# Kernel tuning notes

Hardware: AMD Instinct MI355X
Metric: run time of the kernel (lower is better)

## Reference

```python
import jax, jax.numpy as jnp
import numpy as np

NH = 8  # n_heads
LN_EPS = 1e-5

def _ln(x, g, b):
    m = x.mean(-1, keepdims=True)
    v = ((x - m) ** 2).mean(-1, keepdims=True)
    return (x - m) / jnp.sqrt(v + LN_EPS) * g + b

def _l2norm(x):
    n = jnp.sqrt(jnp.sum(x * x, axis=-1, keepdims=True))
    return x / jnp.maximum(n, 1e-12)

def _block(h, inw, inb, outw, outb, g1, b1, g2, b2, w1, bb1, w2, bb2):
    B, T, D = h.shape
    hd = D // NH
    res = h
    hn = _ln(h, g1, b1)
    qkv = hn @ inw.T + inb
    q, k, v = jnp.split(qkv, 3, axis=-1)
    q = q.reshape(B, T, NH, hd)
    k = k.reshape(B, T, NH, hd)
    v = v.reshape(B, T, NH, hd)
    scores = jnp.einsum('bthd,bshd->bhts', q, k) / jnp.sqrt(jnp.asarray(hd, h.dtype))
    a = jax.nn.softmax(scores, axis=-1)
    o = jnp.einsum('bhts,bshd->bthd', a, v).reshape(B, T, D)
    h = res + o @ outw.T + outb
    f = _ln(h, g2, b2)
    f = jax.nn.gelu(f @ w1.T + bb1, approximate=False) @ w2.T + bb2
    return h + f

def setup_inputs() -> dict:
    B, T, IN, D, L, NS, NP = 8, 1024, 1024, 512, 4, 1024, 512
    key = jax.random.key(0)
    ks = jax.random.split(key, 24)
    gn = jax.random.normal
    u = jax.random.uniform(ks[1], (B, T, NS), dtype=jnp.float32, minval=1e-6, maxval=1.0 - 1e-6)
    gumbel = -jnp.log(-jnp.log(u))
    s = lambda fan: 1.0 / np.sqrt(fan)
    inp = {
        'x': gn(ks[0], (B, T, IN), dtype=jnp.float32),
        'gumbel': gumbel,
        'sym_w': gn(ks[2], (D, IN)) * s(IN),
        'sym_b': jnp.zeros((D,)),
        'codebook': gn(ks[3], (NS, D)) * 0.1,
        'pos_enc': gn(ks[4], (1, 2000, D)) * 0.02,
        'attn_in_w': gn(ks[5], (L, 3 * D, D)) * s(D),
        'attn_in_b': jnp.zeros((L, 3 * D)),
        'attn_out_w': gn(ks[6], (L, D, D)) * s(D),
        'attn_out_b': jnp.zeros((L, D)),
        'n1_g': jnp.ones((L, D)), 'n1_b': jnp.zeros((L, D)),
        'n2_g': jnp.ones((L, D)), 'n2_b': jnp.zeros((L, D)),
        'ffn_w1': gn(ks[7], (L, 4 * D, D)) * s(D),
        'ffn_b1': jnp.zeros((L, 4 * D)),
        'ffn_w2': gn(ks[8], (L, D, 4 * D)) * s(4 * D),
        'ffn_b2': jnp.zeros((L, D)),
        'q_w': gn(ks[9], (D, D)) * s(D),
        'q_b': jnp.zeros((D,)),
        'qln_g': jnp.ones((D,)), 'qln_b': jnp.zeros((D,)),
        'patterns': gn(ks[10], (NP, D)) * s(D),
        'epoch': 0,
        'total_epochs': 100,
    }
    return inp

def reference(x, gumbel, sym_w, sym_b, codebook, pos_enc,
              attn_in_w, attn_in_b, attn_out_w, attn_out_b,
              n1_g, n1_b, n2_g, n2_b, ffn_w1, ffn_b1, ffn_w2, ffn_b2,
              q_w, q_b, qln_g, qln_b, patterns, epoch, total_epochs):
    B, T, _ = x.shape
    # SymbolizationLayer (soft, gumbel-softmax with tau=0.5)
    hp = x @ sym_w.T + sym_b                               # [B,T,D]
    logits_s = _l2norm(hp) @ _l2norm(codebook).T / 0.5     # [B,T,NS]
    soft = jax.nn.softmax((logits_s + gumbel) / 0.5, axis=-1)
    h = soft @ codebook + pos_enc[:, :T, :]
    # transformer blocks
    for i in range(attn_in_w.shape[0]):
        h = _block(h, attn_in_w[i], attn_in_b[i], attn_out_w[i], attn_out_b[i],
                   n1_g[i], n1_b[i], n2_g[i], n2_b[i],
                   ffn_w1[i], ffn_b1[i], ffn_w2[i], ffn_b2[i])
    # VQPatternMatrix (eval mode: hard assignments, no EMA updates)
    Q = _l2norm(_ln(h @ q_w.T + q_b, qln_g, qln_b))
    temp = max(0.5, 1.0 - 0.5 * epoch / total_epochs)
    logits = Q @ _l2norm(patterns).T / temp                # [B,T,NP]
    hard_idx = jnp.argmax(logits, axis=-1)                 # [B,T]
    assign = jax.nn.one_hot(hard_idx, patterns.shape[0], dtype=logits.dtype)
    emb = jnp.take(patterns, hard_idx, axis=0)             # gather = one_hot @ patterns
    return (emb, assign, logits, h, hard_idx)
```

## Files before the change

### kernel.cpp

```cpp
#include <hip/hip_runtime.h>

#define DEV __device__ __forceinline__

typedef unsigned short u16;
typedef unsigned int u32;
typedef __attribute__((ext_vector_type(8))) _Float16 h8_t;
typedef __attribute__((ext_vector_type(4))) float f4_t;

constexpr int T_SEQ = 1024;
constexpr int DMODEL = 512;
constexpr int NPAT = 512;

enum {
  E_BIAS = 0,
  E_VQ = 5,
  E_RES = 6,
  E_ACC = 7,
  E_POS = 8,
  E_GUM2 = 9,
  E_GELU2 = 10,
  E_QKV2 = 11
};

DEV float h2f(u16 h) { return (float)__builtin_bit_cast(_Float16, h); }
DEV void split2(float x, u16& h, u16& l) {
  _Float16 hh = (_Float16)x;
  float r = x - (float)hh;
  _Float16 ll = (_Float16)r;
  h = __builtin_bit_cast(u16, hh);
  l = __builtin_bit_cast(u16, ll);
}

DEV f4_t mfh(h8_t a, h8_t b, f4_t c) {
  return __builtin_amdgcn_mfma_f32_16x16x32_f16(a, b, c, 0, 0, 0);
}
DEV f4_t prod3(h8_t ah, h8_t al, h8_t bh, h8_t bl, f4_t c) {
  c = mfh(ah, bh, c);
  c = mfh(ah, bl, c);
  c = mfh(al, bh, c);
  return c;
}

typedef const __attribute__((address_space(1))) unsigned char* gas_t;
typedef __attribute__((address_space(3))) unsigned char* las_t;
DEV void gload16(const u16* g, u16* l) {
  __builtin_amdgcn_global_load_lds((gas_t)(const void*)g, (las_t)(void*)l, 16,
                                   0, 0);
}

template <int EPI>
__global__ __launch_bounds__(256, 3) void gemm_mf(
    const u16* __restrict__ Ah, const u16* __restrict__ Al,
    const u16* __restrict__ Bh, const u16* __restrict__ Bl,
    const float* __restrict__ bias, const float* __restrict__ res,
    float* __restrict__ Cf, u16* __restrict__ Ch, u16* __restrict__ Cl, int N,
    int KK, int lda, int ldb, int gx) {
  constexpr int BM = 64;
  constexpr int MT = 2;
  __shared__ __align__(16) u16 AsH[2][BM][4][8], AsL[2][BM][4][8];
  __shared__ __align__(16) u16 BsH[2][128][4][8], BsL[2][128][4][8];
  const int tid = threadIdx.x;
  const int w = tid >> 6, lane = tid & 63;
  const int wy = w >> 1, wx = w & 1;
  const int lr = lane & 15, lg = lane >> 4;

  const int nwg = gridDim.x;
  const int bid = blockIdx.x;
  const int qq = nwg >> 3;
  const int wg = (bid & 7) * qq + (bid >> 3);
  const int by = wg / gx, bx = wg % gx;
  const int bm = by * BM, bn = bx * 128;

  const int rowl = lane >> 2, slot4 = lane & 3;

  auto STAGE = [&](int k0, int buf) {
#pragma unroll
    for (int it = 0; it < 2; ++it) {
      const int f = w + 4 * it;
      const int plane = f >> 2;
      const int ch = f & 3;
      const int row = ch * 16 + rowl;
      const int kp = slot4 ^ ((row >> 1) & 3);
      const size_t g = (size_t)(bm + row) * lda + k0 + kp * 8;
      if (plane == 0)
        gload16(&Ah[g], &AsH[buf][0][0][0] + ch * 512);
      else
        gload16(&Al[g], &AsL[buf][0][0][0] + ch * 512);
    }
#pragma unroll
    for (int it = 0; it < 4; ++it) {
      const int f = w + 4 * it;
      const int plane = f >> 3;
      const int ch = f & 7;
      const int row = ch * 16 + rowl;
      const int kp = slot4 ^ ((row >> 1) & 3);
      const size_t g = (size_t)(bn + row) * ldb + k0 + kp * 8;
      if (plane == 0)
        gload16(&Bh[g], &BsH[buf][0][0][0] + ch * 512);
      else
        gload16(&Bl[g], &BsL[buf][0][0][0] + ch * 512);
    }
  };

  f4_t acc[MT][4];
#pragma unroll
  for (int mt = 0; mt < MT; ++mt)
#pragma unroll
    for (int nt = 0; nt < 4; ++nt) acc[mt][nt] = (f4_t){0.f, 0.f, 0.f, 0.f};

  const int nsteps = KK / 32;
  STAGE(0, 0);
  __syncthreads();
  for (int t = 0; t < nsteps; ++t) {
    const int cur = t & 1;
    if (t + 1 < nsteps) STAGE((t + 1) * 32, cur ^ 1);

    h8_t fah[MT], fal[MT], fbh[4], fbl[4];
#pragma unroll
    for (int mt = 0; mt < MT; ++mt) {
      int row = wy * 32 + mt * 16 + lr;
      int slot = lg ^ ((row >> 1) & 3);
      fah[mt] = *(const h8_t*)&AsH[cur][row][slot][0];
      fal[mt] = *(const h8_t*)&AsL[cur][row][slot][0];
    }
#pragma unroll
    for (int nt = 0; nt < 4; ++nt) {
      int col = wx * 64 + nt * 16 + lr;
      int slot = lg ^ ((col >> 1) & 3);
      fbh[nt] = *(const h8_t*)&BsH[cur][col][slot][0];
      fbl[nt] = *(const h8_t*)&BsL[cur][col][slot][0];
    }
#pragma unroll
    for (int mt = 0; mt < MT; ++mt)
#pragma unroll
      for (int nt = 0; nt < 4; ++nt)
        acc[mt][nt] = prod3(fah[mt], fal[mt], fbh[nt], fbl[nt], acc[mt][nt]);
    __syncthreads();
  }

  float bv[4];
  if constexpr (EPI == E_BIAS || EPI == E_RES || EPI == E_GELU2 ||
                EPI == E_QKV2) {
#pragma unroll
    for (int nt = 0; nt < 4; ++nt) bv[nt] = bias[bn + wx * 64 + nt * 16 + lr];
  }
#pragma unroll
  for (int mt = 0; mt < MT; ++mt)
#pragma unroll
    for (int nt = 0; nt < 4; ++nt) {
      const int c = bn + wx * 64 + nt * 16 + lr;
#pragma unroll
      for (int i = 0; i < 4; ++i) {
        const int m = bm + wy * 32 + mt * 16 + 4 * lg + i;
        const size_t idx = (size_t)m * N + c;
        float v = acc[mt][nt][i];
        if constexpr (EPI == E_BIAS) {
          Cf[idx] = v + bv[nt];
        } else if constexpr (EPI == E_RES) {
          Cf[idx] = v + bv[nt] + res[idx];
        } else if constexpr (EPI == E_ACC) {
          Cf[idx] += v;
        } else if constexpr (EPI == E_POS) {
          Cf[idx] = v + res[(size_t)(m & 1023) * N + c];
        } else if constexpr (EPI == E_GUM2) {
          float t = 4.0f * v + 2.0f * res[idx];
          u16 h2, l2;
          split2(t, h2, l2);
          Ch[idx] = h2;
          Cl[idx] = l2;
        } else if constexpr (EPI == E_GELU2) {
          float t = v + bv[nt];
          float g = 0.5f * t * (1.0f + erff(t * 0.7071067811865476f));
          u16 h2, l2;
          split2(g, h2, l2);
          Ch[idx] = h2;
          Cl[idx] = l2;
        } else if constexpr (EPI == E_QKV2) {
          float t = v + bv[nt];
          u16 h2, l2;
          split2(t, h2, l2);
          size_t o;
          if (c < 512) {
            o = (size_t)m * 512 + c;
          } else if (c < 1024) {
            o = 4194304 + (size_t)m * 512 + (c - 512);
          } else {
            int cc = c - 1024, hh2 = cc >> 6, dd = cc & 63;
            int bb2 = m >> 10, tt = m & 1023;
            o = 8388608 +
                (((size_t)(bb2 * 8 + hh2) * 64 + dd) << 10) + tt;
          }
          Ch[o] = h2;
          Cl[o] = l2;
        }
      }
    }
}

__global__ __launch_bounds__(256, 4) void flash_mfma(
    const u16* __restrict__ QKVh, const u16* __restrict__ QKVl,
    u16* __restrict__ Oh, u16* __restrict__ Ol) {
  __shared__ __align__(16) u16 KP[2][64][8][8];
  __shared__ __align__(16) u16 Vs[2][64][8][8];
  const int tid = threadIdx.x;
  const int w = tid >> 6, lane = tid & 63;
  const int lr = lane & 15, lg = lane >> 4;
  const int bid = blockIdx.x;
  const int b = bid & 7;
  const int slot_b = bid >> 3;
  const int hh = slot_b >> 4;
  const int qt = slot_b & 15;

  const u16* Qh = QKVh;
  const u16* Ql = QKVl;
  const u16* Kh = QKVh + 4194304;
  const u16* Kl = QKVl + 4194304;
  const u16* Vh = QKVh + 8388608;
  const u16* Vl = QKVl + 8388608;

  h8_t qf[2][2];
  {
    size_t g =
        ((size_t)(b * 1024 + qt * 64 + w * 16 + lr)) * 512 + hh * 64 + lg * 8;
    qf[0][0] = *(const h8_t*)&Qh[g];
    qf[0][1] = *(const h8_t*)&Ql[g];
    qf[1][0] = *(const h8_t*)&Qh[g + 32];
    qf[1][1] = *(const h8_t*)&Ql[g + 32];
  }

  f4_t oacc[4];
#pragma unroll
  for (int nt = 0; nt < 4; ++nt) oacc[nt] = (f4_t){0.f, 0.f, 0.f, 0.f};
  float mrun[4], lrun[4];
#pragma unroll
  for (int i = 0; i < 4; ++i) {
    mrun[i] = -__builtin_huge_valf();
    lrun[i] = 0.0f;
  }

  const int rowl8 = lane >> 3, slot8 = lane & 7;

  for (int kt = 0; kt < 16; ++kt) {
    __syncthreads();
#pragma unroll
    for (int it = 0; it < 4; ++it) {
      const int f = w + 4 * it;
      const int plane = f >> 3, ch = f & 7;
      const int row = ch * 8 + rowl8;
      const int kp = slot8 ^ (row & 7);
      const size_t gk =
          ((size_t)(b * 1024 + kt * 64 + row)) * 512 + hh * 64 + kp * 8;
      if (plane == 0)
        gload16(&Kh[gk], &KP[0][0][0][0] + ch * 512);
      else
        gload16(&Kl[gk], &KP[1][0][0][0] + ch * 512);
    }
#pragma unroll
    for (int it = 0; it < 4; ++it) {
      const int f = w + 4 * it;
      const int plane = f >> 3, ch = f & 7;
      const int row = ch * 8 + rowl8;
      const int kp = slot8 ^ (row & 7);
      const size_t gv =
          ((size_t)((b * 8 + hh) * 64 + row)) * 1024 + kt * 64 + kp * 8;
      if (plane == 0)
        gload16(&Vh[gv], &Vs[0][0][0][0] + ch * 512);
      else
        gload16(&Vl[gv], &Vs[1][0][0][0] + ch * 512);
    }
    __syncthreads();

    f4_t s[4];
#pragma unroll
    for (int nt = 0; nt < 4; ++nt) {
      s[nt] = (f4_t){0.f, 0.f, 0.f, 0.f};
      const int col = nt * 16 + lr;
#pragma unroll
      for (int ks = 0; ks < 2; ++ks) {
        int slt = (ks * 4 + lg) ^ (col & 7);
        h8_t kh = *(const h8_t*)&KP[0][col][slt][0];
        h8_t kl = *(const h8_t*)&KP[1][col][slt][0];
        s[nt] = prod3(qf[ks][0], qf[ks][1], kh, kl, s[nt]);
      }
    }

#pragma unroll
    for (int i = 0; i < 4; ++i) {
      float rm = -__builtin_huge_valf();
#pragma unroll
      for (int nt = 0; nt < 4; ++nt) {
        s[nt][i] *= 0.125f;
        rm = fmaxf(rm, s[nt][i]);
      }
      rm = fmaxf(rm, __shfl_xor(rm, 1));
      rm = fmaxf(rm, __shfl_xor(rm, 2));
      rm = fmaxf(rm, __shfl_xor(rm, 4));
      rm = fmaxf(rm, __shfl_xor(rm, 8));
      float mnew = fmaxf(mrun[i], rm);
      float alpha = __expf(mrun[i] - mnew);
      float rs = 0.0f;
#pragma unroll
      for (int nt = 0; nt < 4; ++nt) {
        float p = __expf(s[nt][i] - mnew);
        s[nt][i] = p;
        rs += p;
      }
      rs += __shfl_xor(rs, 1);
      rs += __shfl_xor(rs, 2);
      rs += __shfl_xor(rs, 4);
      rs += __shfl_xor(rs, 8);
      lrun[i] = lrun[i] * alpha + rs;
      mrun[i] = mnew;
#pragma unroll
      for (int nt = 0; nt < 4; ++nt) oacc[nt][i] *= alpha;
    }

    __syncthreads();

#pragma unroll
    for (int nt = 0; nt < 4; ++nt)
#pragma unroll
      for (int i = 0; i < 4; ++i) {
        int qrow = w * 16 + 4 * lg + i;
        int kv = nt * 16 + lr;
        int kp = kv >> 3, j = kv & 7;
        int slt = kp ^ (qrow & 7);
        u16 h2, l2;
        split2(s[nt][i], h2, l2);
        KP[0][qrow][slt][j] = h2;
        KP[1][qrow][slt][j] = l2;
      }

    h8_t pf[2][2];
#pragma unroll
    for (int ks = 0; ks < 2; ++ks) {
      int row = w * 16 + lr;
      int slt = (ks * 4 + lg) ^ (row & 7);
      pf[ks][0] = *(const h8_t*)&KP[0][row][slt][0];
      pf[ks][1] = *(const h8_t*)&KP[1][row][slt][0];
    }
#pragma unroll
    for (int ntd = 0; ntd < 4; ++ntd) {
      const int col = ntd * 16 + lr;
#pragma unroll
      for (int ks = 0; ks < 2; ++ks) {
        int slt = (ks * 4 + lg) ^ (col & 7);
        h8_t vh = *(const h8_t*)&Vs[0][col][slt][0];
        h8_t vl = *(const h8_t*)&Vs[1][col][slt][0];
        oacc[ntd] = prod3(pf[ks][0], pf[ks][1], vh, vl, oacc[ntd]);
      }
    }
  }

#pragma unroll
  for (int i = 0; i < 4; ++i) {
    float inv = 1.0f / lrun[i];
    int t = qt * 64 + w * 16 + 4 * lg + i;
#pragma unroll
    for (int ntd = 0; ntd < 4; ++ntd) {
      int d = hh * 64 + ntd * 16 + lr;
      size_t idx = ((size_t)(b * 1024 + t)) * 512 + d;
      u16 h2, l2;
      split2(oacc[ntd][i] * inv, h2, l2);
      Oh[idx] = h2;
      Ol[idx] = l2;
    }
  }
}

template <int BM, int BN, int WR, int EPI>
__global__ __launch_bounds__((BM / WR) * (BN / 64) * 64) void gemm_f32(
    const float* __restrict__ A, const float* __restrict__ Bmat,
    const float* __restrict__ bias, float* __restrict__ C, int M, int N, int K,
    const int* __restrict__ ep, const int* __restrict__ tot) {
  constexpr int BK = 16;
  constexpr int WN = BN / 64;
  constexpr int NW = (BM / WR) * WN;
  constexpr int NT = NW * 64;
  constexpr int RM = WR / 8;
  __shared__ __align__(16) float As[BK][BM + 4];
  __shared__ __align__(16) float Bs[BK][BN + 4];
  const int tid = threadIdx.x;
  const int w = tid >> 6, lane = tid & 63;
  const int wy = w / WN, wx = w % WN;
  const int ly = lane >> 3, lx = lane & 7;
  const int bm = blockIdx.y * BM;
  const int bn = blockIdx.x * BN;
  const int rbase = wy * WR + ly * RM;

  float acc[RM][8];
#pragma unroll
  for (int i = 0; i < RM; ++i)
#pragma unroll
    for (int j = 0; j < 8; ++j) acc[i][j] = 0.0f;

  for (int k0 = 0; k0 < K; k0 += BK) {
#pragma unroll
    for (int i = 0; i < (BM * BK / 4) / NT; ++i) {
      int idx = tid + i * NT;
      int r = idx >> 2, c4 = (idx & 3) << 2;
      const float4 v = *(const float4*)(A + (size_t)(bm + r) * K + k0 + c4);
      As[c4 + 0][r] = v.x;
      As[c4 + 1][r] = v.y;
      As[c4 + 2][r] = v.z;
      As[c4 + 3][r] = v.w;
    }
#pragma unroll
    for (int i = 0; i < (BN * BK / 4) / NT; ++i) {
      int idx = tid + i * NT;
      int r = idx >> 2, c4 = (idx & 3) << 2;
      const float4 v = *(const float4*)(Bmat + (size_t)(bn + r) * K + k0 + c4);
      Bs[c4 + 0][r] = v.x;
      Bs[c4 + 1][r] = v.y;
      Bs[c4 + 2][r] = v.z;
      Bs[c4 + 3][r] = v.w;
    }
    __syncthreads();
#pragma unroll
    for (int k = 0; k < BK; ++k) {
      float a[RM], b[8];
#pragma unroll
      for (int r4 = 0; r4 < RM; r4 += 4)
        *(float4*)&a[r4] = *(const float4*)&As[k][rbase + r4];
      *(float4*)&b[0] = *(const float4*)&Bs[k][wx * 64 + lx * 8];
      *(float4*)&b[4] = *(const float4*)&Bs[k][wx * 64 + lx * 8 + 4];
#pragma unroll
      for (int i = 0; i < RM; ++i)
#pragma unroll
        for (int j = 0; j < 8; ++j) acc[i][j] = fmaf(a[i], b[j], acc[i][j]);
    }
    __syncthreads();
  }

  const int ncol = bn + wx * 64 + lx * 8;
  float bb[8];
  if constexpr (EPI == E_BIAS) {
    *(float4*)&bb[0] = *(const float4*)(bias + ncol);
    *(float4*)&bb[4] = *(const float4*)(bias + ncol + 4);
  }
  float invt = 1.0f;
  if constexpr (EPI == E_VQ) {
    float t = 1.0f - 0.5f * (float)ep[0] / (float)tot[0];
    invt = 1.0f / fmaxf(0.5f, t);
  }
#pragma unroll
  for (int i = 0; i < RM; ++i) {
    const int m = bm + rbase + i;
    float o[8];
#pragma unroll
    for (int j = 0; j < 8; ++j) o[j] = acc[i][j];
    if constexpr (EPI == E_BIAS) {
#pragma unroll
      for (int j = 0; j < 8; ++j) o[j] += bb[j];
    } else if constexpr (EPI == E_VQ) {
#pragma unroll
      for (int j = 0; j < 8; ++j) o[j] *= invt;
    }
    *(float4*)(C + (size_t)m * N + ncol) = *(float4*)&o[0];
    *(float4*)(C + (size_t)m * N + ncol + 4) = *(float4*)&o[4];
  }
}

DEV float wave_sum(float v) {
#pragma unroll
  for (int off = 1; off < 64; off <<= 1) v += __shfl_xor(v, off);
  return v;
}

DEV void store8_split2(u16* H, u16* L, size_t base, const float* t) {
  u16 vh[8], vl[8];
#pragma unroll
  for (int j = 0; j < 8; ++j) split2(t[j], vh[j], vl[j]);
  *(ushort4*)&H[base] = make_ushort4(vh[0], vh[1], vh[2], vh[3]);
  *(ushort4*)&H[base + 4] = make_ushort4(vh[4], vh[5], vh[6], vh[7]);
  *(ushort4*)&L[base] = make_ushort4(vl[0], vl[1], vl[2], vl[3]);
  *(ushort4*)&L[base + 4] = make_ushort4(vl[4], vl[5], vl[6], vl[7]);
}

__global__ __launch_bounds__(256) void ln_split2(const float* __restrict__ x,
                                                 const float* __restrict__ g,
                                                 const float* __restrict__ b,
                                                 u16* __restrict__ yh,
                                                 u16* __restrict__ yl) {
  const int row = blockIdx.x * 4 + (threadIdx.x >> 6);
  const int lane = threadIdx.x & 63;
  const float* xr = x + (size_t)row * DMODEL;
  float v[8];
  *(float4*)&v[0] = *(const float4*)(xr + lane * 8);
  *(float4*)&v[4] = *(const float4*)(xr + lane * 8 + 4);
  float s = 0.0f;
#pragma unroll
  for (int j = 0; j < 8; ++j) s += v[j];
  s = wave_sum(s);
  float mean = s * (1.0f / 512.0f);
  float s2 = 0.0f;
#pragma unroll
  for (int j = 0; j < 8; ++j) {
    float d = v[j] - mean;
    s2 += d * d;
  }
  s2 = wave_sum(s2);
  float rstd = 1.0f / sqrtf(s2 * (1.0f / 512.0f) + 1e-5f);
  float gg[8], bv[8];
  *(float4*)&gg[0] = *(const float4*)(g + lane * 8);
  *(float4*)&gg[4] = *(const float4*)(g + lane * 8 + 4);
  *(float4*)&bv[0] = *(const float4*)(b + lane * 8);
  *(float4*)&bv[4] = *(const float4*)(b + lane * 8 + 4);
  float t[8];
#pragma unroll
  for (int j = 0; j < 8; ++j) t[j] = (v[j] - mean) * rstd * gg[j] + bv[j];
  store8_split2(yh, yl, (size_t)row * DMODEL + lane * 8, t);
}

__global__ __launch_bounds__(256) void ln_l2_f32(const float* __restrict__ x,
                                                 const float* __restrict__ g,
                                                 const float* __restrict__ b,
                                                 float* __restrict__ y) {
  const int row = blockIdx.x * 4 + (threadIdx.x >> 6);
  const int lane = threadIdx.x & 63;
  const float* xr = x + (size_t)row * DMODEL;
  float v[8];
  *(float4*)&v[0] = *(const float4*)(xr + lane * 8);
  *(float4*)&v[4] = *(const float4*)(xr + lane * 8 + 4);
  float s = 0.0f;
#pragma unroll
  for (int j = 0; j < 8; ++j) s += v[j];
  s = wave_sum(s);
  float mean = s * (1.0f / 512.0f);
  float s2 = 0.0f;
#pragma unroll
  for (int j = 0; j < 8; ++j) {
    float d = v[j] - mean;
    s2 += d * d;
  }
  s2 = wave_sum(s2);
  float rstd = 1.0f / sqrtf(s2 * (1.0f / 512.0f) + 1e-5f);
  float gg[8], bv[8];
  *(float4*)&gg[0] = *(const float4*)(g + lane * 8);
  *(float4*)&gg[4] = *(const float4*)(g + lane * 8 + 4);
  *(float4*)&bv[0] = *(const float4*)(b + lane * 8);
  *(float4*)&bv[4] = *(const float4*)(b + lane * 8 + 4);
  float t[8];
#pragma unroll
  for (int j = 0; j < 8; ++j) t[j] = (v[j] - mean) * rstd * gg[j] + bv[j];
  float n2 = 0.0f;
#pragma unroll
  for (int j = 0; j < 8; ++j) n2 += t[j] * t[j];
  n2 = wave_sum(n2);
  float den = fmaxf(sqrtf(n2), 1e-12f);
#pragma unroll
  for (int j = 0; j < 8; ++j) t[j] /= den;
  float* yr = y + (size_t)row * DMODEL;
  *(float4*)(yr + lane * 8) = *(float4*)&t[0];
  *(float4*)(yr + lane * 8 + 4) = *(float4*)&t[4];
}

__global__ __launch_bounds__(256) void l2_split2(const float* __restrict__ x,
                                                 u16* __restrict__ yh,
                                                 u16* __restrict__ yl) {
  const int row = blockIdx.x * 4 + (threadIdx.x >> 6);
  const int lane = threadIdx.x & 63;
  const float* xr = x + (size_t)row * DMODEL;
  float v[8];
  *(float4*)&v[0] = *(const float4*)(xr + lane * 8);
  *(float4*)&v[4] = *(const float4*)(xr + lane * 8 + 4);
  float n2 = 0.0f;
#pragma unroll
  for (int j = 0; j < 8; ++j) n2 += v[j] * v[j];
  n2 = wave_sum(n2);
  float den = fmaxf(sqrtf(n2), 1e-12f);
#pragma unroll
  for (int j = 0; j < 8; ++j) v[j] /= den;
  store8_split2(yh, yl, (size_t)row * DMODEL + lane * 8, v);
}

__global__ __launch_bounds__(256) void l2_f32(const float* __restrict__ x,
                                              float* __restrict__ y) {
  const int row = blockIdx.x * 4 + (threadIdx.x >> 6);
  const int lane = threadIdx.x & 63;
  const float* xr = x + (size_t)row * DMODEL;
  float v[8];
  *(float4*)&v[0] = *(const float4*)(xr + lane * 8);
  *(float4*)&v[4] = *(const float4*)(xr + lane * 8 + 4);
  float n2 = 0.0f;
#pragma unroll
  for (int j = 0; j < 8; ++j) n2 += v[j] * v[j];
  n2 = wave_sum(n2);
  float den = fmaxf(sqrtf(n2), 1e-12f);
#pragma unroll
  for (int j = 0; j < 8; ++j) v[j] /= den;
  float* yr = y + (size_t)row * DMODEL;
  *(float4*)(yr + lane * 8) = *(float4*)&v[0];
  *(float4*)(yr + lane * 8 + 4) = *(float4*)&v[4];
}

__global__ __launch_bounds__(256) void softmax2(u16* __restrict__ H,
                                                u16* __restrict__ L) {
  const int row = blockIdx.x;
  const int tid = threadIdx.x;
  const size_t base = (size_t)row * 1024 + tid * 4;
  ushort4 qh = *(const ushort4*)&H[base];
  ushort4 ql = *(const ushort4*)&L[base];
  float v0 = h2f(qh.x) + h2f(ql.x);
  float v1 = h2f(qh.y) + h2f(ql.y);
  float v2 = h2f(qh.z) + h2f(ql.z);
  float v3 = h2f(qh.w) + h2f(ql.w);
  float mx = fmaxf(fmaxf(v0, v1), fmaxf(v2, v3));
#pragma unroll
  for (int off = 1; off < 64; off <<= 1) mx = fmaxf(mx, __shfl_xor(mx, off));
  __shared__ float red[4];
  const int wv = tid >> 6;
  if ((tid & 63) == 0) red[wv] = mx;
  __syncthreads();
  mx = fmaxf(fmaxf(red[0], red[1]), fmaxf(red[2], red[3]));
  float e0 = __expf(v0 - mx), e1 = __expf(v1 - mx), e2 = __expf(v2 - mx),
        e3 = __expf(v3 - mx);
  float s = e0 + e1 + e2 + e3;
#pragma unroll
  for (int off = 1; off < 64; off <<= 1) s += __shfl_xor(s, off);
  __syncthreads();
  if ((tid & 63) == 0) red[wv] = s;
  __syncthreads();
  s = red[0] + red[1] + red[2] + red[3];
  float inv = 1.0f / s;
  u16 ah[4], al[4];
  split2(e0 * inv, ah[0], al[0]);
  split2(e1 * inv, ah[1], al[1]);
  split2(e2 * inv, ah[2], al[2]);
  split2(e3 * inv, ah[3], al[3]);
  *(ushort4*)&H[base] = make_ushort4(ah[0], ah[1], ah[2], ah[3]);
  *(ushort4*)&L[base] = make_ushort4(al[0], al[1], al[2], al[3]);
}

__global__ __launch_bounds__(256) void split2_k(const float* __restrict__ src,
                                                u16* __restrict__ H,
                                                u16* __restrict__ L, int n4) {
  for (int e = blockIdx.x * 256 + threadIdx.x; e < n4; e += gridDim.x * 256) {
    float4 v = *(const float4*)(src + (size_t)e * 4);
    u16 ah[4], al[4];
    split2(v.x, ah[0], al[0]);
    split2(v.y, ah[1], al[1]);
    split2(v.z, ah[2], al[2]);
    split2(v.w, ah[3], al[3]);
    *(ushort4*)&H[(size_t)e * 4] = make_ushort4(ah[0], ah[1], ah[2], ah[3]);
    *(ushort4*)&L[(size_t)e * 4] = make_ushort4(al[0], al[1], al[2], al[3]);
  }
}

__global__ __launch_bounds__(256) void tsplit_cb(const float* __restrict__ cb,
                                                 u16* __restrict__ th,
                                                 u16* __restrict__ tl) {
  const int c = blockIdx.x;
  const int t = threadIdx.x;
  u16 ah[4], al[4];
#pragma unroll
  for (int j = 0; j < 4; ++j) {
    float v = cb[(size_t)(4 * t + j) * 512 + c];
    split2(v, ah[j], al[j]);
  }
  const size_t base = (size_t)c * 1024 + 4 * t;
  *(ushort4*)&th[base] = make_ushort4(ah[0], ah[1], ah[2], ah[3]);
  *(ushort4*)&tl[base] = make_ushort4(al[0], al[1], al[2], al[3]);
}

__global__ __launch_bounds__(256) void vq_finalize(
    const float* __restrict__ logits, const float* __restrict__ patterns,
    float* __restrict__ emb, float* __restrict__ assign,
    float* __restrict__ idxf) {
  const int row = blockIdx.x * 4 + (threadIdx.x >> 6);
  const int lane = threadIdx.x & 63;
  const float* lr = logits + (size_t)row * NPAT;
  float best = -__builtin_huge_valf();
  int bi = 0;
#pragma unroll
  for (int jj = 0; jj < 8; ++jj) {
    int j = lane + jj * 64;
    float v = lr[j];
    if (v > best) {
      best = v;
      bi = j;
    }
  }
#pragma unroll
  for (int off = 1; off < 64; off <<= 1) {
    float ob = __shfl_xor(best, off);
    int oi = __shfl_xor(bi, off);
    if (ob > best || (ob == best && oi < bi)) {
      best = ob;
      bi = oi;
    }
  }
  const float* pr = patterns + (size_t)bi * DMODEL;
#pragma unroll
  for (int g = 0; g < 2; ++g) {
    int c = lane * 8 + g * 4;
    float4 pv = *(const float4*)(pr + c);
    *(float4*)(emb + (size_t)row * DMODEL + c) = pv;
    float4 av;
    av.x = (c + 0 == bi) ? 1.0f : 0.0f;
    av.y = (c + 1 == bi) ? 1.0f : 0.0f;
    av.z = (c + 2 == bi) ? 1.0f : 0.0f;
    av.w = (c + 3 == bi) ? 1.0f : 0.0f;
    *(float4*)(assign + (size_t)row * NPAT + c) = av;
  }
  if (lane == 0) idxf[row] = (float)bi;
}

extern "C" void kernel_launch(void* const* d_in, const int* in_sizes, int n_in,
                              void* d_out, int out_size, void* d_ws,
                              size_t ws_size, hipStream_t stream) {
  (void)in_sizes;
  (void)n_in;
  (void)out_size;
  (void)ws_size;
  const float* x = (const float*)d_in[0];
  const float* gumbel = (const float*)d_in[1];
  const float* sym_w = (const float*)d_in[2];
  const float* sym_b = (const float*)d_in[3];
  const float* codebook = (const float*)d_in[4];
  const float* pos_enc = (const float*)d_in[5];
  const float* attn_in_w = (const float*)d_in[6];
  const float* attn_in_b = (const float*)d_in[7];
  const float* attn_out_w = (const float*)d_in[8];
  const float* attn_out_b = (const float*)d_in[9];
  const float* n1_g = (const float*)d_in[10];
  const float* n1_b = (const float*)d_in[11];
  const float* n2_g = (const float*)d_in[12];
  const float* n2_b = (const float*)d_in[13];
  const float* ffn_w1 = (const float*)d_in[14];
  const float* ffn_b1 = (const float*)d_in[15];
  const float* ffn_w2 = (const float*)d_in[16];
  const float* ffn_b2 = (const float*)d_in[17];
  const float* q_w = (const float*)d_in[18];
  const float* q_b = (const float*)d_in[19];
  const float* qln_g = (const float*)d_in[20];
  const float* qln_b = (const float*)d_in[21];
  const float* patterns = (const float*)d_in[22];
  const int* epoch = (const int*)d_in[23];
  const int* tot = (const int*)d_in[24];

  float* out = (float*)d_out;
  float* emb = out;
  float* assign = out + 4194304;
  float* logits = out + 8388608;
  float* h = out + 12582912;
  float* idxf = out + 16777216;

  float* ws_f = (float*)d_ws;
  u16* a16 = (u16*)ws_f;
  float* bF = ws_f + 18874368;
  u16* b16 = (u16*)bF;
  u16 *hnH = b16, *hnL = b16 + 4194304;
  float* wF = ws_f + 25165824;
  u16* w16 = (u16*)wF;

  u16 *xH = a16, *xL = a16 + 8388608;
  split2_k<<<2048, 256, 0, stream>>>(x, xH, xL, 2097152);
  split2_k<<<512, 256, 0, stream>>>(sym_w, w16, w16 + 524288, 131072);
  gemm_mf<E_BIAS><<<512, 256, 0, stream>>>(xH, xL, w16, w16 + 524288, sym_b,
                                           nullptr, bF, nullptr, nullptr, 512,
                                           1024, 1024, 1024, 4);
  l2_split2<<<256, 256, 0, stream>>>(codebook, w16, w16 + 524288);
  u16 *hpH = a16, *hpL = a16 + 4194304;
  l2_split2<<<2048, 256, 0, stream>>>(bF, hpH, hpL);
  u16 *sH = a16 + 12582912, *sL = a16 + 20971520;
  gemm_mf<E_GUM2><<<1024, 256, 0, stream>>>(hpH, hpL, w16, w16 + 524288,
                                            nullptr, gumbel, nullptr, sH, sL,
                                            1024, 512, 512, 512, 8);
  softmax2<<<8192, 256, 0, stream>>>(sH, sL);
  tsplit_cb<<<512, 256, 0, stream>>>(codebook, w16, w16 + 524288);
  gemm_mf<E_POS><<<512, 256, 0, stream>>>(sH, sL, w16, w16 + 524288, nullptr,
                                          pos_enc, h, nullptr, nullptr, 512,
                                          1024, 1024, 1024, 4);

  u16 *qkvH = a16, *qkvL = a16 + 12582912;
  u16* w1p = (u16*)(ws_f + 12582912);
  u16* w2p = (u16*)(ws_f + 13631488);
  u16 *pH = a16, *pL = a16 + 8388608;

  for (int l = 0; l < 4; ++l) {
    const float* inw = attn_in_w + (size_t)l * 1536 * 512;
    const float* inb = attn_in_b + (size_t)l * 1536;
    const float* outw = attn_out_w + (size_t)l * 512 * 512;
    const float* outb = attn_out_b + (size_t)l * 512;
    const float* w1 = ffn_w1 + (size_t)l * 2048 * 512;
    const float* b1 = ffn_b1 + (size_t)l * 2048;
    const float* w2 = ffn_w2 + (size_t)l * 512 * 2048;
    const float* b2 = ffn_b2 + (size_t)l * 512;

    ln_split2<<<2048, 256, 0, stream>>>(h, n1_g + l * 512, n1_b + l * 512,
                                        hnH, hnL);
    split2_k<<<1024, 256, 0, stream>>>(inw, w16, w16 + 786432, 196608);
    gemm_mf<E_QKV2><<<1536, 256, 0, stream>>>(hnH, hnL, w16, w16 + 786432,
                                              inb, nullptr, nullptr, qkvH,
                                              qkvL, 1536, 512, 512, 512, 12);
    flash_mfma<<<1024, 256, 0, stream>>>(qkvH, qkvL, hnH, hnL);
    split2_k<<<256, 256, 0, stream>>>(outw, w16, w16 + 262144, 65536);
    gemm_mf<E_RES><<<512, 256, 0, stream>>>(hnH, hnL, w16, w16 + 262144, outb,
                                            h, h, nullptr, nullptr, 512, 512,
                                            512, 512, 4);
    ln_split2<<<2048, 256, 0, stream>>>(h, n2_g + l * 512, n2_b + l * 512,
                                        hnH, hnL);
    split2_k<<<1024, 256, 0, stream>>>(w1, w1p, w1p + 1048576, 262144);
    split2_k<<<1024, 256, 0, stream>>>(w2, w2p, w2p + 1048576, 262144);
    for (int c = 0; c < 2; ++c) {
      gemm_mf<E_GELU2><<<1024, 256, 0, stream>>>(
          hnH, hnL, w1p + c * 524288, w1p + 1048576 + c * 524288, b1 + c * 1024,
          nullptr, nullptr, pH, pL, 1024, 512, 512, 512, 8);
      if (c == 0) {
        gemm_mf<E_RES><<<512, 256, 0, stream>>>(
            pH, pL, w2p + 0, w2p + 1048576, b2, h, h, nullptr, nullptr, 512,
            1024, 1024, 2048, 4);
      } else {
        gemm_mf<E_ACC><<<512, 256, 0, stream>>>(
            pH, pL, w2p + 1024, w2p + 1048576 + 1024, nullptr, nullptr, h,
            nullptr, nullptr, 512, 1024, 1024, 2048, 4);
      }
    }
  }

  gemm_f32<64, 128, 32, E_BIAS><<<dim3(4, 128), 256, 0, stream>>>(
      h, q_w, q_b, bF, 8192, 512, 512, nullptr, nullptr);
  ln_l2_f32<<<2048, 256, 0, stream>>>(bF, qln_g, qln_b, bF);
  l2_f32<<<128, 256, 0, stream>>>(patterns, wF);
  gemm_f32<64, 128, 32, E_VQ><<<dim3(4, 128), 256, 0, stream>>>(
      bF, wF, nullptr, logits, 8192, 512, 512, epoch, tot);
  vq_finalize<<<2048, 256, 0, stream>>>(logits, patterns, emb, assign, idxf);
}
```

Before: 1.805 ms.

## Enlarge GEMM tile to 128x128 and merge split FFN GEMMs into single launches

The MFMA GEMM tile grows from 64x128 to 128x128, so each wave computes a 4x4 grid of 16x16 fragments. Grid sizes are halved, the launch-bounds occupancy hint drops from 3 to 2 workgroups, and A-tile reuse rises while global loads per output fall. The FFN no longer splits the hidden dimension into two halves. It runs one GELU GEMM over all 2048 columns and one full-K down-projection with a residual epilogue, which removes the accumulate pass and its extra read-modify-write of h. Workspace pointers move to hold the larger intermediate, and the accumulate epilogue is deleted. Register pressure rises and occupancy falls, and the smaller grids (256 blocks) may underfill the GPU.

```diff
diff --git a/kernel.cpp b/kernel.cpp
--- a/kernel.cpp
+++ b/kernel.cpp
@@ -15,7 +15,6 @@
   E_BIAS = 0,
   E_VQ = 5,
   E_RES = 6,
-  E_ACC = 7,
   E_POS = 8,
   E_GUM2 = 9,
   E_GELU2 = 10,
@@ -49,15 +48,13 @@
 }
 
 template <int EPI>
-__global__ __launch_bounds__(256, 3) void gemm_mf(
+__global__ __launch_bounds__(256, 2) void gemm_mf(
     const u16* __restrict__ Ah, const u16* __restrict__ Al,
     const u16* __restrict__ Bh, const u16* __restrict__ Bl,
     const float* __restrict__ bias, const float* __restrict__ res,
     float* __restrict__ Cf, u16* __restrict__ Ch, u16* __restrict__ Cl, int N,
     int KK, int lda, int ldb, int gx) {
-  constexpr int BM = 64;
-  constexpr int MT = 2;
-  __shared__ __align__(16) u16 AsH[2][BM][4][8], AsL[2][BM][4][8];
+  __shared__ __align__(16) u16 AsH[2][128][4][8], AsL[2][128][4][8];
   __shared__ __align__(16) u16 BsH[2][128][4][8], BsL[2][128][4][8];
   const int tid = threadIdx.x;
   const int w = tid >> 6, lane = tid & 63;
@@ -69,16 +66,16 @@
   const int qq = nwg >> 3;
   const int wg = (bid & 7) * qq + (bid >> 3);
   const int by = wg / gx, bx = wg % gx;
-  const int bm = by * BM, bn = bx * 128;
+  const int bm = by * 128, bn = bx * 128;
 
   const int rowl = lane >> 2, slot4 = lane & 3;
 
   auto STAGE = [&](int k0, int buf) {
 #pragma unroll
-    for (int it = 0; it < 2; ++it) {
+    for (int it = 0; it < 4; ++it) {
       const int f = w + 4 * it;
-      const int plane = f >> 2;
-      const int ch = f & 3;
+      const int plane = f >> 3;
+      const int ch = f & 7;
       const int row = ch * 16 + rowl;
       const int kp = slot4 ^ ((row >> 1) & 3);
       const size_t g = (size_t)(bm + row) * lda + k0 + kp * 8;
@@ -102,9 +99,9 @@
     }
   };
 
-  f4_t acc[MT][4];
-#pragma unroll
-  for (int mt = 0; mt < MT; ++mt)
+  f4_t acc[4][4];
+#pragma unroll
+  for (int mt = 0; mt < 4; ++mt)
 #pragma unroll
     for (int nt = 0; nt < 4; ++nt) acc[mt][nt] = (f4_t){0.f, 0.f, 0.f, 0.f};
 
@@ -115,10 +112,10 @@
     const int cur = t & 1;
     if (t + 1 < nsteps) STAGE((t + 1) * 32, cur ^ 1);
 
-    h8_t fah[MT], fal[MT], fbh[4], fbl[4];
-#pragma unroll
-    for (int mt = 0; mt < MT; ++mt) {
-      int row = wy * 32 + mt * 16 + lr;
+    h8_t fah[4], fal[4], fbh[4], fbl[4];
+#pragma unroll
+    for (int mt = 0; mt < 4; ++mt) {
+      int row = wy * 64 + mt * 16 + lr;
       int slot = lg ^ ((row >> 1) & 3);
       fah[mt] = *(const h8_t*)&AsH[cur][row][slot][0];
       fal[mt] = *(const h8_t*)&AsL[cur][row][slot][0];
@@ -131,7 +128,7 @@
       fbl[nt] = *(const h8_t*)&BsL[cur][col][slot][0];
     }
 #pragma unroll
-    for (int mt = 0; mt < MT; ++mt)
+    for (int mt = 0; mt < 4; ++mt)
 #pragma unroll
       for (int nt = 0; nt < 4; ++nt)
         acc[mt][nt] = prod3(fah[mt], fal[mt], fbh[nt], fbl[nt], acc[mt][nt]);
@@ -145,21 +142,19 @@
     for (int nt = 0; nt < 4; ++nt) bv[nt] = bias[bn + wx * 64 + nt * 16 + lr];
   }
 #pragma unroll
-  for (int mt = 0; mt < MT; ++mt)
+  for (int mt = 0; mt < 4; ++mt)
 #pragma unroll
     for (int nt = 0; nt < 4; ++nt) {
       const int c = bn + wx * 64 + nt * 16 + lr;
 #pragma unroll
       for (int i = 0; i < 4; ++i) {
-        const int m = bm + wy * 32 + mt * 16 + 4 * lg + i;
+        const int m = bm + wy * 64 + mt * 16 + 4 * lg + i;
         const size_t idx = (size_t)m * N + c;
         float v = acc[mt][nt][i];
         if constexpr (EPI == E_BIAS) {
           Cf[idx] = v + bv[nt];
         } else if constexpr (EPI == E_RES) {
           Cf[idx] = v + bv[nt] + res[idx];
-        } else if constexpr (EPI == E_ACC) {
-          Cf[idx] += v;
         } else if constexpr (EPI == E_POS) {
           Cf[idx] = v + res[(size_t)(m & 1023) * N + c];
         } else if constexpr (EPI == E_GUM2) {
@@ -757,26 +752,26 @@
   u16 *xH = a16, *xL = a16 + 8388608;
   split2_k<<<2048, 256, 0, stream>>>(x, xH, xL, 2097152);
   split2_k<<<512, 256, 0, stream>>>(sym_w, w16, w16 + 524288, 131072);
-  gemm_mf<E_BIAS><<<512, 256, 0, stream>>>(xH, xL, w16, w16 + 524288, sym_b,
+  gemm_mf<E_BIAS><<<256, 256, 0, stream>>>(xH, xL, w16, w16 + 524288, sym_b,
                                            nullptr, bF, nullptr, nullptr, 512,
                                            1024, 1024, 1024, 4);
   l2_split2<<<256, 256, 0, stream>>>(codebook, w16, w16 + 524288);
   u16 *hpH = a16, *hpL = a16 + 4194304;
   l2_split2<<<2048, 256, 0, stream>>>(bF, hpH, hpL);
   u16 *sH = a16 + 12582912, *sL = a16 + 20971520;
-  gemm_mf<E_GUM2><<<1024, 256, 0, stream>>>(hpH, hpL, w16, w16 + 524288,
-                                            nullptr, gumbel, nullptr, sH, sL,
-                                            1024, 512, 512, 512, 8);
+  gemm_mf<E_GUM2><<<512, 256, 0, stream>>>(hpH, hpL, w16, w16 + 524288,
+                                           nullptr, gumbel, nullptr, sH, sL,
+                                           1024, 512, 512, 512, 8);
   softmax2<<<8192, 256, 0, stream>>>(sH, sL);
   tsplit_cb<<<512, 256, 0, stream>>>(codebook, w16, w16 + 524288);
-  gemm_mf<E_POS><<<512, 256, 0, stream>>>(sH, sL, w16, w16 + 524288, nullptr,
+  gemm_mf<E_POS><<<256, 256, 0, stream>>>(sH, sL, w16, w16 + 524288, nullptr,
                                           pos_enc, h, nullptr, nullptr, 512,
                                           1024, 1024, 1024, 4);
 
   u16 *qkvH = a16, *qkvL = a16 + 12582912;
-  u16* w1p = (u16*)(ws_f + 12582912);
-  u16* w2p = (u16*)(ws_f + 13631488);
-  u16 *pH = a16, *pL = a16 + 8388608;
+  u16* w1p = a16 + 33554432;
+  u16* w2p = b16 + 8388608;
+  u16 *pH = a16, *pL = a16 + 16777216;
 
   for (int l = 0; l < 4; ++l) {
     const float* inw = attn_in_w + (size_t)l * 1536 * 512;
@@ -791,32 +786,24 @@
     ln_split2<<<2048, 256, 0, stream>>>(h, n1_g + l * 512, n1_b + l * 512,
                                         hnH, hnL);
     split2_k<<<1024, 256, 0, stream>>>(inw, w16, w16 + 786432, 196608);
-    gemm_mf<E_QKV2><<<1536, 256, 0, stream>>>(hnH, hnL, w16, w16 + 786432,
-                                              inb, nullptr, nullptr, qkvH,
-                                              qkvL, 1536, 512, 512, 512, 12);
+    gemm_mf<E_QKV2><<<768, 256, 0, stream>>>(hnH, hnL, w16, w16 + 786432, inb,
+                                             nullptr, nullptr, qkvH, qkvL,
+                                             1536, 512, 512, 512, 12);
     flash_mfma<<<1024, 256, 0, stream>>>(qkvH, qkvL, hnH, hnL);
     split2_k<<<256, 256, 0, stream>>>(outw, w16, w16 + 262144, 65536);
-    gemm_mf<E_RES><<<512, 256, 0, stream>>>(hnH, hnL, w16, w16 + 262144, outb,
+    gemm_mf<E_RES><<<256, 256, 0, stream>>>(hnH, hnL, w16, w16 + 262144, outb,
                                             h, h, nullptr, nullptr, 512, 512,
                                             512, 512, 4);
     ln_split2<<<2048, 256, 0, stream>>>(h, n2_g + l * 512, n2_b + l * 512,
                                         hnH, hnL);
     split2_k<<<1024, 256, 0, stream>>>(w1, w1p, w1p + 1048576, 262144);
     split2_k<<<1024, 256, 0, stream>>>(w2, w2p, w2p + 1048576, 262144);
-    for (int c = 0; c < 2; ++c) {
-      gemm_mf<E_GELU2><<<1024, 256, 0, stream>>>(
-          hnH, hnL, w1p + c * 524288, w1p + 1048576 + c * 524288, b1 + c * 1024,
-          nullptr, nullptr, pH, pL, 1024, 512, 512, 512, 8);
-      if (c == 0) {
-        gemm_mf<E_RES><<<512, 256, 0, stream>>>(
-            pH, pL, w2p + 0, w2p + 1048576, b2, h, h, nullptr, nullptr, 512,
-            1024, 1024, 2048, 4);
-      } else {
-        gemm_mf<E_ACC><<<512, 256, 0, stream>>>(
-            pH, pL, w2p + 1024, w2p + 1048576 + 1024, nullptr, nullptr, h,
-            nullptr, nullptr, 512, 1024, 1024, 2048, 4);
-      }
-    }
+    gemm_mf<E_GELU2><<<1024, 256, 0, stream>>>(hnH, hnL, w1p, w1p + 1048576,
+                                               b1, nullptr, nullptr, pH, pL,
+                                               2048, 512, 512, 512, 16);
+    gemm_mf<E_RES><<<256, 256, 0, stream>>>(pH, pL, w2p, w2p + 1048576, b2, h,
+                                            h, nullptr, nullptr, 512, 2048,
+                                            2048, 2048, 4);
   }
 
   gemm_f32<64, 128, 32, E_BIAS><<<dim3(4, 128), 256, 0, stream>>>(
```

New measurement: 1.766 ms. 2.2% less time.
